# Kernel optimization log

Measured on AMD Instinct MI355X. Metric: run time of the kernel, lower is better.

Reference implementation:

```python
import jax, jax.numpy as jnp
import numpy as np

# SNNConfig defaults
TAU_MEM_INV = 1.0 / 10.0
TAU_SYN_INV = 1.0 / 5.0
V_TH = 1.0
V_RESET = 0.0
V_LEAK = 0.0
DT = 1.0


def setup_inputs() -> dict:
    key = jax.random.key(0)
    k1, k2 = jax.random.split(key)
    B, T, I, H = 32, 2048, 512, 1024
    x = jax.random.normal(k1, (B, T, I), dtype=jnp.float32)
    # nn.Linear default init scale ~ 1/sqrt(fan_in)
    W = jax.random.normal(k2, (H, I), dtype=jnp.float32) * (1.0 / np.sqrt(I))
    b = jnp.zeros((H,), dtype=jnp.float32)
    return {"x": x, "W": W, "b": b}


def reference(x, W, b):
    """SNNBackend._forward_sequence with Norse lif_step semantics.

    x: [B, T, I]; W: [H, I]; b: [H]. Returns (spikes [B,T,H], v_final, i_final).
    """
    # input_proj applied to every timestep (one big GEMM instead of per-step)
    current = jnp.einsum('bti,hi->bth', x, W) + b  # [B, T, H]
    B, T, H = current.shape
    v0 = jnp.zeros((B, H), dtype=x.dtype)
    i0 = jnp.zeros((B, H), dtype=x.dtype)

    def step(carry, c_t):
        v, i = carry
        # membrane/synaptic integration (Norse lif_step)
        v_dec = v + DT * TAU_MEM_INV * ((V_LEAK - v) + i)
        i_dec = i + DT * (-TAU_SYN_INV) * i
        z = (v_dec - V_TH > 0).astype(v.dtype)  # spike
        v_new = (1.0 - z) * v_dec + z * V_RESET  # reset
        i_new = i_dec + c_t  # inject input current
        return (v_new, i_new), z

    (v_f, i_f), spikes_t = jax.lax.scan(step, (v0, i0), jnp.swapaxes(current, 0, 1))
    spikes = jnp.swapaxes(spikes_t, 0, 1)  # [B, T, H]
    return spikes, v_f, i_f
```

## Files before the change

### kernel.cpp

```cpp
#include <hip/hip_runtime.h>


static constexpr int BM = 128, BN = 128, BK = 16;

__global__ __launch_bounds__(256) void snn_gemm_f32(
    const float* __restrict__ X,
    const float* __restrict__ Wt,
    const float* __restrict__ bias,
    float* __restrict__ C,
    int M, int N, int K)
{
    __shared__ float As[2][BK][BM + 4];
    __shared__ float Bs[2][BK][BN + 4];

    const int tid   = threadIdx.x;
    const int mBase = blockIdx.y * BM;
    const int nBase = blockIdx.x * BN;

    const int row0 = tid >> 2;
    const int kq   = (tid & 3) * 4;
    const int row1 = row0 + 64;

    const int tx = tid & 15;
    const int ty = tid >> 4;

    const float* Xp = X + (size_t)mBase * K;
    const float* Wp = Wt + (size_t)nBase * K;

    float acc[8][8];
#pragma unroll
    for (int i = 0; i < 8; ++i)
#pragma unroll
        for (int j = 0; j < 8; ++j) acc[i][j] = 0.f;

    float4 ra0, ra1, rb0, rb1;

    ra0 = *(const float4*)(Xp + (size_t)row0 * K + kq);
    ra1 = *(const float4*)(Xp + (size_t)row1 * K + kq);
    rb0 = *(const float4*)(Wp + (size_t)row0 * K + kq);
    rb1 = *(const float4*)(Wp + (size_t)row1 * K + kq);

    As[0][kq + 0][row0] = ra0.x; As[0][kq + 1][row0] = ra0.y;
    As[0][kq + 2][row0] = ra0.z; As[0][kq + 3][row0] = ra0.w;
    As[0][kq + 0][row1] = ra1.x; As[0][kq + 1][row1] = ra1.y;
    As[0][kq + 2][row1] = ra1.z; As[0][kq + 3][row1] = ra1.w;
    Bs[0][kq + 0][row0] = rb0.x; Bs[0][kq + 1][row0] = rb0.y;
    Bs[0][kq + 2][row0] = rb0.z; Bs[0][kq + 3][row0] = rb0.w;
    Bs[0][kq + 0][row1] = rb1.x; Bs[0][kq + 1][row1] = rb1.y;
    Bs[0][kq + 2][row1] = rb1.z; Bs[0][kq + 3][row1] = rb1.w;
    __syncthreads();

    const int nk = K / BK;
#pragma unroll 1
    for (int kt = 0; kt < nk; ++kt) {
        const int cur = kt & 1;
        if (kt + 1 < nk) {
            const int k0 = (kt + 1) * BK;
            ra0 = *(const float4*)(Xp + (size_t)row0 * K + k0 + kq);
            ra1 = *(const float4*)(Xp + (size_t)row1 * K + k0 + kq);
            rb0 = *(const float4*)(Wp + (size_t)row0 * K + k0 + kq);
            rb1 = *(const float4*)(Wp + (size_t)row1 * K + k0 + kq);
        }
#pragma unroll
        for (int kk = 0; kk < BK; ++kk) {
            float a[8], bv[8];
            *(float4*)&a[0]  = *(const float4*)&As[cur][kk][ty * 4];
            *(float4*)&a[4]  = *(const float4*)&As[cur][kk][ty * 4 + 64];
            *(float4*)&bv[0] = *(const float4*)&Bs[cur][kk][tx * 4];
            *(float4*)&bv[4] = *(const float4*)&Bs[cur][kk][tx * 4 + 64];
#pragma unroll
            for (int i = 0; i < 8; ++i)
#pragma unroll
                for (int j = 0; j < 8; ++j)
                    acc[i][j] = fmaf(a[i], bv[j], acc[i][j]);
        }
        if (kt + 1 < nk) {
            const int nxt = cur ^ 1;
            As[nxt][kq + 0][row0] = ra0.x; As[nxt][kq + 1][row0] = ra0.y;
            As[nxt][kq + 2][row0] = ra0.z; As[nxt][kq + 3][row0] = ra0.w;
            As[nxt][kq + 0][row1] = ra1.x; As[nxt][kq + 1][row1] = ra1.y;
            As[nxt][kq + 2][row1] = ra1.z; As[nxt][kq + 3][row1] = ra1.w;
            Bs[nxt][kq + 0][row0] = rb0.x; Bs[nxt][kq + 1][row0] = rb0.y;
            Bs[nxt][kq + 2][row0] = rb0.z; Bs[nxt][kq + 3][row0] = rb0.w;
            Bs[nxt][kq + 0][row1] = rb1.x; Bs[nxt][kq + 1][row1] = rb1.y;
            Bs[nxt][kq + 2][row1] = rb1.z; Bs[nxt][kq + 3][row1] = rb1.w;
        }
        __syncthreads();
    }

    const float4 bb0 = *(const float4*)(bias + nBase + tx * 4);
    const float4 bb1 = *(const float4*)(bias + nBase + tx * 4 + 64);
#pragma unroll
    for (int i = 0; i < 8; ++i) {
        const int m = mBase + ty * 4 + (i & 3) + ((i >> 2) << 6);
        float4 o0, o1;
        o0.x = acc[i][0] + bb0.x; o0.y = acc[i][1] + bb0.y;
        o0.z = acc[i][2] + bb0.z; o0.w = acc[i][3] + bb0.w;
        o1.x = acc[i][4] + bb1.x; o1.y = acc[i][5] + bb1.y;
        o1.z = acc[i][6] + bb1.z; o1.w = acc[i][7] + bb1.w;
        *(float4*)(C + (size_t)m * N + nBase + tx * 4)      = o0;
        *(float4*)(C + (size_t)m * N + nBase + tx * 4 + 64) = o1;
    }
}

__global__ __launch_bounds__(64) void snn_scan(
    const float* cur, float* spk, float* vf, float* iff,
    int T, int H)
{
    const int idx = blockIdx.x * blockDim.x + threadIdx.x;
    const int h = idx & (H - 1);
    const int b = idx >> 10;
    const size_t base = ((size_t)b * T) * H + h;

    constexpr int U = 32;
    float ca[U];
#pragma unroll
    for (int j = 0; j < U; ++j) ca[j] = cur[base + (size_t)j * H];

    float v = 0.f, ii = 0.f;
    for (int t0 = 0; t0 < T; t0 += U) {
        float cb[U];
        const bool pref = (t0 + U) < T;
#pragma unroll
        for (int j = 0; j < U; ++j)
            cb[j] = pref ? cur[base + (size_t)(t0 + U + j) * H] : 0.f;
#pragma unroll
        for (int j = 0; j < U; ++j) {
            const float v_dec = v + 0.1f * ((0.0f - v) + ii);
            const float i_dec = ii - 0.2f * ii;
            const float z = (v_dec > 1.0f) ? 1.0f : 0.0f;
            v  = (v_dec > 1.0f) ? 0.0f : v_dec;
            ii = i_dec + ca[j];
            spk[base + (size_t)(t0 + j) * H] = z;
        }
#pragma unroll
        for (int j = 0; j < U; ++j) ca[j] = cb[j];
    }
    vf[idx]  = v;
    iff[idx] = ii;
}

extern "C" void kernel_launch(void* const* d_in, const int* in_sizes, int n_in,
                              void* d_out, int out_size, void* d_ws, size_t ws_size,
                              hipStream_t stream) {
    const int B = 32, T = 2048, I = 512, H = 1024;
    const int M = B * T, N = H, K = I;

    const float* x    = (const float*)d_in[0];
    const float* W    = (const float*)d_in[1];
    const float* bias = (const float*)d_in[2];

    float* out    = (float*)d_out;
    float* spikes = out;
    float* vf     = out + (size_t)B * T * H;
    float* iff    = vf + (size_t)B * H;

    const size_t curBytes = (size_t)B * T * H * sizeof(float);
    float* curbuf = (ws_size >= curBytes) ? (float*)d_ws : spikes;

    dim3 grid(N / BN, M / BM);
    snn_gemm_f32<<<grid, 256, 0, stream>>>(x, W, bias, curbuf, M, N, K);

    const int nNeuron = B * H;
    snn_scan<<<nNeuron / 64, 64, 0, stream>>>(curbuf, spikes, vf, iff, T, H);
}
```

Baseline: 1.493 ms.

## Load W operand directly from global into registers, drop B shared tile

The GEMM no longer stages the weight tile in shared memory. Each thread reads its 8 weight rows as float4 vectors straight from global memory (expected to hit L1/L2) and keeps only X in LDS. This removes half of the LDS stores and reads and frees shared memory, at the cost of strided, less coalesced global loads per thread and more register pressure. The scan kernel's prefetch unroll is also halved from 32 to 16.

```diff
diff --git a/kernel.cpp b/kernel.cpp
--- a/kernel.cpp
+++ b/kernel.cpp
@@ -11,21 +11,22 @@
     int M, int N, int K)
 {
     __shared__ float As[2][BK][BM + 4];
-    __shared__ float Bs[2][BK][BN + 4];
 
     const int tid   = threadIdx.x;
     const int mBase = blockIdx.y * BM;
     const int nBase = blockIdx.x * BN;
 
-    const int row0 = tid >> 2;
-    const int kq   = (tid & 3) * 4;
-    const int row1 = row0 + 64;
+    const int lrow = tid >> 2;
+    const int lkq  = (tid & 3) << 2;
 
     const int tx = tid & 15;
     const int ty = tid >> 4;
 
-    const float* Xp = X + (size_t)mBase * K;
-    const float* Wp = Wt + (size_t)nBase * K;
+    const float* Xp = X + (size_t)(mBase + lrow) * K + lkq;
+    const size_t Xrow64 = (size_t)64 * K;
+
+    const float* wp0 = Wt + (size_t)(nBase + tx * 4) * K;
+    const float* wp1 = wp0 + (size_t)64 * K;
 
     float acc[8][8];
 #pragma unroll
@@ -33,57 +34,62 @@
 #pragma unroll
         for (int j = 0; j < 8; ++j) acc[i][j] = 0.f;
 
-    float4 ra0, ra1, rb0, rb1;
+    float4 ra0, ra1;
 
-    ra0 = *(const float4*)(Xp + (size_t)row0 * K + kq);
-    ra1 = *(const float4*)(Xp + (size_t)row1 * K + kq);
-    rb0 = *(const float4*)(Wp + (size_t)row0 * K + kq);
-    rb1 = *(const float4*)(Wp + (size_t)row1 * K + kq);
-
-    As[0][kq + 0][row0] = ra0.x; As[0][kq + 1][row0] = ra0.y;
-    As[0][kq + 2][row0] = ra0.z; As[0][kq + 3][row0] = ra0.w;
-    As[0][kq + 0][row1] = ra1.x; As[0][kq + 1][row1] = ra1.y;
-    As[0][kq + 2][row1] = ra1.z; As[0][kq + 3][row1] = ra1.w;
-    Bs[0][kq + 0][row0] = rb0.x; Bs[0][kq + 1][row0] = rb0.y;
-    Bs[0][kq + 2][row0] = rb0.z; Bs[0][kq + 3][row0] = rb0.w;
-    Bs[0][kq + 0][row1] = rb1.x; Bs[0][kq + 1][row1] = rb1.y;
-    Bs[0][kq + 2][row1] = rb1.z; Bs[0][kq + 3][row1] = rb1.w;
+    ra0 = *(const float4*)(Xp);
+    ra1 = *(const float4*)(Xp + Xrow64);
+    As[0][lkq + 0][lrow] = ra0.x; As[0][lkq + 1][lrow] = ra0.y;
+    As[0][lkq + 2][lrow] = ra0.z; As[0][lkq + 3][lrow] = ra0.w;
+    As[0][lkq + 0][lrow + 64] = ra1.x; As[0][lkq + 1][lrow + 64] = ra1.y;
+    As[0][lkq + 2][lrow + 64] = ra1.z; As[0][lkq + 3][lrow + 64] = ra1.w;
     __syncthreads();
 
     const int nk = K / BK;
 #pragma unroll 1
     for (int kt = 0; kt < nk; ++kt) {
         const int cur = kt & 1;
-        if (kt + 1 < nk) {
+        const bool more = (kt + 1) < nk;
+        if (more) {
             const int k0 = (kt + 1) * BK;
-            ra0 = *(const float4*)(Xp + (size_t)row0 * K + k0 + kq);
-            ra1 = *(const float4*)(Xp + (size_t)row1 * K + k0 + kq);
-            rb0 = *(const float4*)(Wp + (size_t)row0 * K + k0 + kq);
-            rb1 = *(const float4*)(Wp + (size_t)row1 * K + k0 + kq);
+            ra0 = *(const float4*)(Xp + k0);
+            ra1 = *(const float4*)(Xp + k0 + Xrow64);
         }
+
+        const float (*as)[BM + 4] = As[cur];
+        const int kbase = kt * BK;
+
 #pragma unroll
-        for (int kk = 0; kk < BK; ++kk) {
-            float a[8], bv[8];
-            *(float4*)&a[0]  = *(const float4*)&As[cur][kk][ty * 4];
-            *(float4*)&a[4]  = *(const float4*)&As[cur][kk][ty * 4 + 64];
-            *(float4*)&bv[0] = *(const float4*)&Bs[cur][kk][tx * 4];
-            *(float4*)&bv[4] = *(const float4*)&Bs[cur][kk][tx * 4 + 64];
+        for (int g = 0; g < 4; ++g) {
+            float4 bq[8];
 #pragma unroll
-            for (int i = 0; i < 8; ++i)
+            for (int r = 0; r < 4; ++r) {
+                bq[r]     = *(const float4*)(wp0 + (size_t)r * K + kbase + g * 4);
+                bq[r + 4] = *(const float4*)(wp1 + (size_t)r * K + kbase + g * 4);
+            }
+#pragma unroll
+            for (int kk = 0; kk < 4; ++kk) {
+                float a[8];
+                *(float4*)&a[0] = *(const float4*)&as[g * 4 + kk][ty * 4];
+                *(float4*)&a[4] = *(const float4*)&as[g * 4 + kk][ty * 4 + 64];
+                float bv[8];
 #pragma unroll
                 for (int j = 0; j < 8; ++j)
-                    acc[i][j] = fmaf(a[i], bv[j], acc[i][j]);
+                    bv[j] = (kk == 0) ? bq[j].x : (kk == 1) ? bq[j].y
+                          : (kk == 2) ? bq[j].z : bq[j].w;
+#pragma unroll
+                for (int i = 0; i < 8; ++i)
+#pragma unroll
+                    for (int j = 0; j < 8; ++j)
+                        acc[i][j] = fmaf(a[i], bv[j], acc[i][j]);
+            }
         }
-        if (kt + 1 < nk) {
+
+        if (more) {
             const int nxt = cur ^ 1;
-            As[nxt][kq + 0][row0] = ra0.x; As[nxt][kq + 1][row0] = ra0.y;
-            As[nxt][kq + 2][row0] = ra0.z; As[nxt][kq + 3][row0] = ra0.w;
-            As[nxt][kq + 0][row1] = ra1.x; As[nxt][kq + 1][row1] = ra1.y;
-            As[nxt][kq + 2][row1] = ra1.z; As[nxt][kq + 3][row1] = ra1.w;
-            Bs[nxt][kq + 0][row0] = rb0.x; Bs[nxt][kq + 1][row0] = rb0.y;
-            Bs[nxt][kq + 2][row0] = rb0.z; Bs[nxt][kq + 3][row0] = rb0.w;
-            Bs[nxt][kq + 0][row1] = rb1.x; Bs[nxt][kq + 1][row1] = rb1.y;
-            Bs[nxt][kq + 2][row1] = rb1.z; Bs[nxt][kq + 3][row1] = rb1.w;
+            As[nxt][lkq + 0][lrow] = ra0.x; As[nxt][lkq + 1][lrow] = ra0.y;
+            As[nxt][lkq + 2][lrow] = ra0.z; As[nxt][lkq + 3][lrow] = ra0.w;
+            As[nxt][lkq + 0][lrow + 64] = ra1.x; As[nxt][lkq + 1][lrow + 64] = ra1.y;
+            As[nxt][lkq + 2][lrow + 64] = ra1.z; As[nxt][lkq + 3][lrow + 64] = ra1.w;
         }
         __syncthreads();
     }
@@ -112,7 +118,7 @@
     const int b = idx >> 10;
     const size_t base = ((size_t)b * T) * H + h;
 
-    constexpr int U = 32;
+    constexpr int U = 16;
     float ca[U];
 #pragma unroll
     for (int j = 0; j < U; ++j) ca[j] = cur[base + (size_t)j * H];
```

Measured after the change: 2.774 ms. 1.86x slower.
